# Performance work log

Measured on AMD Instinct MI355X. Metric: run time of the kernel, lower is better.

Reference implementation:

```python
import jax, jax.numpy as jnp
import numpy as np

B, S, H = 2, 2048, 4096          # batch, seq_len, hidden_size
NH, NKV, D = 32, 8, 128          # query heads, kv heads (GQA), head_dim
WINDOW = 1024                    # sliding window size
EPS = 1e-5
THETA = 10000.0


def setup_inputs() -> dict:
    key = jax.random.key(0)
    ks = jax.random.split(key, 5)
    w = lambda k, shape: jax.random.normal(k, shape, jnp.float32) * 0.02
    return {
        "hidden_states": jax.random.normal(ks[0], (B, S, H), jnp.float32),
        "wq": w(ks[1], (H, NH * D)),
        "wk": w(ks[2], (H, NKV * D)),
        "wv": w(ks[3], (H, NKV * D)),
        "wo": w(ks[4], (NH * D, H)),
        "q_norm_w": jnp.ones((D,), jnp.float32),
        "k_norm_w": jnp.ones((D,), jnp.float32),
    }


def _rmsnorm(x, w):
    # Exaone4RMSNorm over the last (head_dim) axis
    var = jnp.mean(jnp.square(x.astype(jnp.float32)), axis=-1, keepdims=True)
    return (x * jax.lax.rsqrt(var + EPS)).astype(x.dtype) * w


def _rotate_half(x):
    x1, x2 = jnp.split(x, 2, axis=-1)
    return jnp.concatenate([-x2, x1], axis=-1)


def reference(hidden_states, wq, wk, wv, wo, q_norm_w, k_norm_w):
    # QKV projections (no bias)
    q = (hidden_states @ wq).reshape(B, S, NH, D)
    k = (hidden_states @ wk).reshape(B, S, NKV, D)
    v = (hidden_states @ wv).reshape(B, S, NKV, D)
    # per-head QK RMSNorm, then [B, h, S, D] layout
    q = _rmsnorm(q, q_norm_w).transpose(0, 2, 1, 3)
    k = _rmsnorm(k, k_norm_w).transpose(0, 2, 1, 3)
    v = v.transpose(0, 2, 1, 3)
    # RoPE (applied on sliding-window layers in EXAONE4)
    pos = jnp.arange(S)
    inv_freq = 1.0 / (THETA ** (jnp.arange(0, D, 2, dtype=jnp.float32) / D))
    freqs = pos[:, None].astype(jnp.float32) * inv_freq[None, :]   # [S, D/2]
    emb = jnp.concatenate([freqs, freqs], axis=-1)                 # [S, D]
    cos, sin = jnp.cos(emb), jnp.sin(emb)
    q = q * cos + _rotate_half(q) * sin
    k = k * cos + _rotate_half(k) * sin
    # GQA: repeat kv heads to match query heads
    k = jnp.repeat(k, NH // NKV, axis=1)
    v = jnp.repeat(v, NH // NKV, axis=1)
    # SDPA with causal sliding-window mask: q_pos - WINDOW < k_pos <= q_pos
    scores = jnp.einsum('bhqd,bhkd->bhqk', q, k) / jnp.sqrt(jnp.float32(D))
    diff = pos[:, None] - pos[None, :]
    mask = (diff >= 0) & (diff < WINDOW)
    scores = jnp.where(mask, scores, jnp.finfo(scores.dtype).min)
    probs = jax.nn.softmax(scores, axis=-1)
    out = jnp.einsum('bhqk,bhkd->bhqd', probs, v)
    out = out.transpose(0, 2, 1, 3).reshape(B, S, NH * D)
    return out @ wo
```

## Files before the change

### kernel.cpp

```cpp
#include <hip/hip_runtime.h>
#include <hip/hip_bf16.h>

#define B_ 2
#define S_ 2048
#define H_ 4096
#define NH_ 32
#define NKV_ 8
#define D_ 128
#define WINDOW_ 1024
#define EPS_ 1e-5f
#define M_ (B_*S_)
#define NQKV_ ((NH_ + 2*NKV_) * D_)

typedef __attribute__((ext_vector_type(8))) __bf16 bf16x8;
typedef __attribute__((ext_vector_type(4))) float f32x4;
typedef __attribute__((ext_vector_type(16))) float f32x16;

__device__ __forceinline__ unsigned short f2bf(float f) {
  union { __hip_bfloat16 h; unsigned short us; } cv;
  cv.h = __float2bfloat16(f);
  return cv.us;
}
__device__ __forceinline__ float bf2f(unsigned short u) {
  union { __hip_bfloat16 h; unsigned short us; } cv;
  cv.us = u;
  return __bfloat162float(cv.h);
}

__device__ __forceinline__ void gload16(const unsigned short* g, unsigned short* l) {
  __builtin_amdgcn_global_load_lds(
      (const __attribute__((address_space(1))) unsigned int*)(const void*)g,
      (__attribute__((address_space(3))) unsigned int*)(void*)l, 16, 0, 0);
}

__global__ __launch_bounds__(256) void transpose_convert(
    const float* __restrict__ in, unsigned short* __restrict__ out, int K, int N) {
  __shared__ float tile[32][33];
  const int n0 = blockIdx.x * 32, k0 = blockIdx.y * 32;
  const int t = threadIdx.x;
  #pragma unroll
  for (int i = 0; i < 4; ++i) {
    int e = i * 256 + t; int r = e >> 5, c = e & 31;
    tile[r][c] = in[(size_t)(k0 + r) * N + n0 + c];
  }
  __syncthreads();
  #pragma unroll
  for (int i = 0; i < 4; ++i) {
    int e = i * 256 + t; int r = e >> 5, c = e & 31;
    out[(size_t)(n0 + r) * K + k0 + c] = f2bf(tile[c][r]);
  }
}

__global__ __launch_bounds__(256) void convert_bf16_kernel(
    const float* __restrict__ in, unsigned short* __restrict__ out, int n4) {
  int i = blockIdx.x * 256 + threadIdx.x;
  if (i >= n4) return;
  float4 v = ((const float4*)in)[i];
  ushort4 o;
  o.x = f2bf(v.x); o.y = f2bf(v.y); o.z = f2bf(v.z); o.w = f2bf(v.w);
  ((ushort4*)out)[i] = o;
}

template <bool OUT_BF16>
__global__ __launch_bounds__(512) void gemm9(
    const unsigned short* __restrict__ A, const unsigned short* __restrict__ Bt,
    void* __restrict__ Cout, int N, int K) {
  __shared__ __align__(16) unsigned short lds[2][2][16384];
  const int tid = threadIdx.x;
  const int wave = tid >> 6, lane = tid & 63;
  const int l15 = lane & 15, l16 = lane >> 4;
  const int m0 = blockIdx.y * 256, n0 = blockIdx.x * 256;
  const int wmi = wave >> 2, wni = wave & 3;

  const unsigned short* asrc[4];
  const unsigned short* bsrc[4];
  #pragma unroll
  for (int it = 0; it < 4; ++it) {
    const int d = it * 512 + tid;
    const int row = d >> 3, cis = (d & 7) ^ (row & 7);
    asrc[it] = A + (size_t)(m0 + row) * K + cis * 8;
    bsrc[it] = Bt + (size_t)(n0 + row) * K + cis * 8;
  }

  int offA[2][8], offB[2][4];
  #pragma unroll
  for (int kk = 0; kk < 2; ++kk) {
    #pragma unroll
    for (int mi = 0; mi < 8; ++mi) {
      const int row = wmi * 128 + mi * 16 + l15;
      offA[kk][mi] = row * 64 + ((kk * 4 + l16) ^ (row & 7)) * 8;
    }
    #pragma unroll
    for (int ni = 0; ni < 4; ++ni) {
      const int row = wni * 64 + ni * 16 + l15;
      offB[kk][ni] = row * 64 + ((kk * 4 + l16) ^ (row & 7)) * 8;
    }
  }

  f32x4 acc[8][4];
  #pragma unroll
  for (int mi = 0; mi < 8; ++mi)
    #pragma unroll
    for (int ni = 0; ni < 4; ++ni) acc[mi][ni] = (f32x4){0.f, 0.f, 0.f, 0.f};

#define STG(buf, kt)                                                         \
  { _Pragma("unroll") for (int it = 0; it < 4; ++it) {                       \
      const int dst = it * 4096 + wave * 512;                                \
      gload16(asrc[it] + (size_t)(kt) * 64, &lds[buf][0][dst]);              \
      gload16(bsrc[it] + (size_t)(kt) * 64, &lds[buf][1][dst]);              \
    } }

#define PHASE_MFMA(MOFF)                                                     \
  asm volatile("s_waitcnt lgkmcnt(0)" ::: "memory");                         \
  __builtin_amdgcn_sched_barrier(0);                                         \
  __builtin_amdgcn_s_setprio(1);                                             \
  _Pragma("unroll") for (int i = 0; i < 4; ++i)                              \
    _Pragma("unroll") for (int j = 0; j < 4; ++j)                            \
      acc[(MOFF) + i][j] = __builtin_amdgcn_mfma_f32_16x16x32_bf16(          \
          av[i], bv[j], acc[(MOFF) + i][j], 0, 0, 0);                        \
  __builtin_amdgcn_s_setprio(0);                                             \
  __builtin_amdgcn_sched_barrier(0);

  const int nk = K >> 6;
  STG(0, 0)
  for (int t = 0; t < nk; ++t) {
    const int cur = t & 1;
    if (t + 1 < nk) {
      STG(cur ^ 1, t + 1)
      asm volatile("s_waitcnt vmcnt(8)" ::: "memory");
    } else {
      asm volatile("s_waitcnt vmcnt(0)" ::: "memory");
    }
    __builtin_amdgcn_sched_barrier(0);
    __builtin_amdgcn_s_barrier();
    __builtin_amdgcn_sched_barrier(0);
    const unsigned short* as = lds[cur][0];
    const unsigned short* bs = lds[cur][1];
    bf16x8 av[4], bv[4];
    #pragma unroll
    for (int i = 0; i < 4; ++i) av[i] = *(const bf16x8*)&as[offA[0][i]];
    #pragma unroll
    for (int j = 0; j < 4; ++j) bv[j] = *(const bf16x8*)&bs[offB[0][j]];
    PHASE_MFMA(0)
    __builtin_amdgcn_s_barrier();
    #pragma unroll
    for (int i = 0; i < 4; ++i) av[i] = *(const bf16x8*)&as[offA[0][i + 4]];
    PHASE_MFMA(4)
    __builtin_amdgcn_s_barrier();
    #pragma unroll
    for (int i = 0; i < 4; ++i) av[i] = *(const bf16x8*)&as[offA[1][i]];
    #pragma unroll
    for (int j = 0; j < 4; ++j) bv[j] = *(const bf16x8*)&bs[offB[1][j]];
    PHASE_MFMA(0)
    __builtin_amdgcn_s_barrier();
    #pragma unroll
    for (int i = 0; i < 4; ++i) av[i] = *(const bf16x8*)&as[offA[1][i + 4]];
    PHASE_MFMA(4)
    __builtin_amdgcn_s_barrier();
    __builtin_amdgcn_sched_barrier(0);
  }
#undef STG
#undef PHASE_MFMA

  #pragma unroll
  for (int mi = 0; mi < 8; ++mi) {
    #pragma unroll
    for (int ni = 0; ni < 4; ++ni) {
      const int col = n0 + wni * 64 + ni * 16 + l15;
      #pragma unroll
      for (int j = 0; j < 4; ++j) {
        const int row = m0 + wmi * 128 + mi * 16 + l16 * 4 + j;
        if (OUT_BF16)
          ((unsigned short*)Cout)[(size_t)row * N + col] = f2bf(acc[mi][ni][j]);
        else
          ((float*)Cout)[(size_t)row * N + col] = acc[mi][ni][j];
      }
    }
  }
}

__global__ __launch_bounds__(256) void norm_rope_kernel(
    const unsigned short* __restrict__ QKVg,
    const float* __restrict__ qw, const float* __restrict__ kw,
    unsigned short* __restrict__ Qr, unsigned short* __restrict__ Kr) {
  const int bs = blockIdx.x;
  const int b = bs >> 11, s = bs & (S_ - 1);
  const int wave = threadIdx.x >> 6, lane = threadIdx.x & 63;

  float invf = 1.0f / powf(10000.0f, (float)lane * (1.0f / 64.0f));
  float sn, cs;
  sincosf((float)s * invf, &sn, &cs);

  const unsigned short* row = QKVg + (size_t)bs * NQKV_;
  const float qwa = qw[lane], qwb = qw[lane + 64];
  const float kwa = kw[lane], kwb = kw[lane + 64];
  const float scale = 0.08838834764831845f;

  for (int h = wave; h < NH_; h += 4) {
    float x0 = bf2f(row[h * D_ + lane]);
    float x1 = bf2f(row[h * D_ + 64 + lane]);
    float ss = x0 * x0 + x1 * x1;
    #pragma unroll
    for (int o = 32; o >= 1; o >>= 1) ss += __shfl_xor(ss, o);
    float r = rsqrtf(ss * (1.0f / 128.0f) + EPS_);
    x0 *= r * qwa; x1 *= r * qwb;
    float o0 = (x0 * cs - x1 * sn) * scale;
    float o1 = (x1 * cs + x0 * sn) * scale;
    size_t off = (((size_t)b * NH_ + h) * S_ + s) * D_;
    Qr[off + lane] = f2bf(o0);
    Qr[off + 64 + lane] = f2bf(o1);
  }
  for (int h = wave; h < NKV_; h += 4) {
    float x0 = bf2f(row[NH_ * D_ + h * D_ + lane]);
    float x1 = bf2f(row[NH_ * D_ + h * D_ + 64 + lane]);
    float ss = x0 * x0 + x1 * x1;
    #pragma unroll
    for (int o = 32; o >= 1; o >>= 1) ss += __shfl_xor(ss, o);
    float r = rsqrtf(ss * (1.0f / 128.0f) + EPS_);
    x0 *= r * kwa; x1 *= r * kwb;
    float o0 = x0 * cs - x1 * sn;
    float o1 = x1 * cs + x0 * sn;
    size_t off = (((size_t)b * NKV_ + h) * S_ + s) * D_;
    Kr[off + lane] = f2bf(o0);
    Kr[off + 64 + lane] = f2bf(o1);
  }
}

__global__ __launch_bounds__(256) void vtrans_kernel(
    const unsigned short* __restrict__ QKVg, unsigned short* __restrict__ Vt) {
  __shared__ unsigned short t[64][65];
  const int s0 = blockIdx.x * 64, d0 = blockIdx.y * 64;
  const int bh = blockIdx.z;
  const int b = bh >> 3, hk = bh & 7;
  const int tid = threadIdx.x;
  #pragma unroll
  for (int i = 0; i < 16; ++i) {
    int e = i * 256 + tid; int sr = e >> 6, dc = e & 63;
    t[sr][dc] = QKVg[(size_t)(b * S_ + s0 + sr) * NQKV_ + (NH_ + NKV_) * D_ + hk * D_ + d0 + dc];
  }
  __syncthreads();
  #pragma unroll
  for (int i = 0; i < 16; ++i) {
    int e = i * 256 + tid; int dr = e >> 6, sc = e & 63;
    Vt[((size_t)bh * D_ + d0 + dr) * S_ + s0 + sc] = t[sc][dr];
  }
}

__global__ __launch_bounds__(512) void attn_kernel(
    const unsigned short* __restrict__ Qr, const unsigned short* __restrict__ Kr,
    const unsigned short* __restrict__ Vt, unsigned short* __restrict__ Out) {
  const int q0 = blockIdx.x * 256;
  const int h = blockIdx.y, b = blockIdx.z, hk = h >> 2;
  const int tid = threadIdx.x;
  const int wave = tid >> 6, lane = tid & 63;
  const int l31 = lane & 31, hi = lane >> 5;
  const int qw0 = q0 + wave * 32;
  const int qpos = qw0 + l31;

  __shared__ __align__(16) unsigned short Ks[64 * 128];
  __shared__ __align__(16) unsigned short Vs[128 * 64];

  bf16x8 qf[8];
  {
    const unsigned short* qp = Qr + (((size_t)b * NH_ + h) * S_ + qpos) * D_ + hi * 8;
    #pragma unroll
    for (int ds = 0; ds < 8; ++ds) qf[ds] = *(const bf16x8*)(qp + ds * 16);
  }

  f32x16 o[4];
  #pragma unroll
  for (int i = 0; i < 4; ++i)
    #pragma unroll
    for (int j = 0; j < 16; ++j) o[i][j] = 0.f;
  float mrun = -1e30f, lrun = 0.f;

  const size_t kbase = ((size_t)b * NKV_ + hk) * S_;
  const size_t vbase = ((size_t)b * NKV_ + hk) * D_;

  const int ktlo = (q0 > 1023) ? ((q0 - 1023) & ~63) : 0;
  const int kthi = (q0 + 255) & ~63;
  const int wlo = (qw0 > 1023) ? ((qw0 - 1023) & ~63) : 0;
  const int whi = (qw0 + 31) & ~63;

  for (int kt = ktlo; kt <= kthi; kt += 64) {
    __syncthreads();
    #pragma unroll
    for (int it = 0; it < 2; ++it) {
      const int cb = it * 512 + wave * 64;
      const int c = cb + lane;
      const int rk = c >> 4, sk = c & 15;
      gload16(Kr + (kbase + kt + rk) * D_ + ((sk ^ (rk & 7)) * 8), Ks + (size_t)cb * 8);
      const int rv = c >> 3, sv = c & 7;
      gload16(Vt + (vbase + rv) * S_ + kt + ((sv ^ (rv & 7)) * 8), Vs + (size_t)cb * 8);
    }
    __syncthreads();
    if (kt < wlo || kt > whi) continue;

    f32x16 s0, s1;
    #pragma unroll
    for (int j = 0; j < 16; ++j) { s0[j] = 0.f; s1[j] = 0.f; }
    __builtin_amdgcn_s_setprio(1);
    #pragma unroll
    for (int ds = 0; ds < 8; ++ds) {
      const int g = ((ds * 2 + hi) ^ (l31 & 7)) * 8;
      bf16x8 k0 = *(const bf16x8*)&Ks[l31 * 128 + g];
      bf16x8 k1 = *(const bf16x8*)&Ks[(l31 + 32) * 128 + g];
      s0 = __builtin_amdgcn_mfma_f32_32x32x16_bf16(k0, qf[ds], s0, 0, 0, 0);
      s1 = __builtin_amdgcn_mfma_f32_32x32x16_bf16(k1, qf[ds], s1, 0, 0, 0);
    }
    __builtin_amdgcn_s_setprio(0);

    const bool fullValid = (kt + 63 <= qw0) && (kt >= qw0 - 992);
    if (!fullValid) {
      const int d0 = qpos - kt;
      #pragma unroll
      for (int r = 0; r < 16; ++r) {
        const int koff = (r & 3) + 8 * (r >> 2) + 4 * hi;
        if ((unsigned)(d0 - koff) >= (unsigned)WINDOW_) s0[r] = -1e30f;
        if ((unsigned)(d0 - koff - 32) >= (unsigned)WINDOW_) s1[r] = -1e30f;
      }
    }

    float pm = -1e30f;
    #pragma unroll
    for (int r = 0; r < 16; ++r) pm = fmaxf(pm, fmaxf(s0[r], s1[r]));
    pm = fmaxf(pm, __shfl_xor(pm, 32));
    const float mnew = fmaxf(mrun, pm);
    const float scl = __expf(mrun - mnew);
    mrun = mnew;
    float ts = 0.f;
    #pragma unroll
    for (int r = 0; r < 16; ++r) {
      s0[r] = __expf(s0[r] - mnew); ts += s0[r];
      s1[r] = __expf(s1[r] - mnew); ts += s1[r];
    }
    ts += __shfl_xor(ts, 32);
    lrun = lrun * scl + ts;
    #pragma unroll
    for (int i = 0; i < 4; ++i)
      #pragma unroll
      for (int j = 0; j < 16; ++j) o[i][j] *= scl;

    unsigned pw[2][2][4];
    #pragma unroll
    for (int t2 = 0; t2 < 2; ++t2) {
      const f32x16 sv = t2 ? s1 : s0;
      #pragma unroll
      for (int sub = 0; sub < 2; ++sub) {
        const int bs4 = sub * 8;
        unsigned A0 = ((unsigned)f2bf(sv[bs4 + 1]) << 16) | f2bf(sv[bs4 + 0]);
        unsigned A1 = ((unsigned)f2bf(sv[bs4 + 3]) << 16) | f2bf(sv[bs4 + 2]);
        unsigned B0 = ((unsigned)f2bf(sv[bs4 + 5]) << 16) | f2bf(sv[bs4 + 4]);
        unsigned B1 = ((unsigned)f2bf(sv[bs4 + 7]) << 16) | f2bf(sv[bs4 + 6]);
        unsigned sA0 = __shfl_xor(A0, 32), sA1 = __shfl_xor(A1, 32);
        unsigned sB0 = __shfl_xor(B0, 32), sB1 = __shfl_xor(B1, 32);
        pw[t2][sub][0] = hi ? sB0 : A0;
        pw[t2][sub][1] = hi ? sB1 : A1;
        pw[t2][sub][2] = hi ? B0 : sA0;
        pw[t2][sub][3] = hi ? B1 : sA1;
      }
    }

    __builtin_amdgcn_s_setprio(1);
    #pragma unroll
    for (int t2 = 0; t2 < 2; ++t2)
      #pragma unroll
      for (int sub = 0; sub < 2; ++sub) {
        union { unsigned u[4]; bf16x8 v; } pb;
        pb.u[0] = pw[t2][sub][0]; pb.u[1] = pw[t2][sub][1];
        pb.u[2] = pw[t2][sub][2]; pb.u[3] = pw[t2][sub][3];
        #pragma unroll
        for (int dt = 0; dt < 4; ++dt) {
          const int rr = dt * 32 + l31;
          const int g = ((t2 * 4 + sub * 2 + hi) ^ (rr & 7)) * 8;
          bf16x8 vf = *(const bf16x8*)&Vs[rr * 64 + g];
          o[dt] = __builtin_amdgcn_mfma_f32_32x32x16_bf16(vf, pb.v, o[dt], 0, 0, 0);
        }
      }
    __builtin_amdgcn_s_setprio(0);
  }

  const float inv = 1.0f / lrun;
  unsigned short* op = Out + (size_t)(b * S_ + qpos) * (NH_ * D_) + h * D_;
  #pragma unroll
  for (int dt = 0; dt < 4; ++dt)
    #pragma unroll
    for (int g = 0; g < 4; ++g) {
      const int r = g * 4;
      uint2 val;
      val.x = ((unsigned)f2bf(o[dt][r + 1] * inv) << 16) | f2bf(o[dt][r + 0] * inv);
      val.y = ((unsigned)f2bf(o[dt][r + 3] * inv) << 16) | f2bf(o[dt][r + 2] * inv);
      *(uint2*)(op + dt * 32 + 8 * g + 4 * hi) = val;
    }
}

extern "C" void kernel_launch(void* const* d_in, const int* in_sizes, int n_in,
                              void* d_out, int out_size, void* d_ws, size_t ws_size,
                              hipStream_t stream) {
  const float* hidden = (const float*)d_in[0];
  const float* wq = (const float*)d_in[1];
  const float* wk = (const float*)d_in[2];
  const float* wv = (const float*)d_in[3];
  const float* wo = (const float*)d_in[4];
  const float* qw = (const float*)d_in[5];
  const float* kw = (const float*)d_in[6];
  float* out = (float*)d_out;

  char* ws = (char*)d_ws;
  unsigned short* wqkv = (unsigned short*)(ws);
  unsigned short* kr   = (unsigned short*)(ws);
  unsigned short* vt   = (unsigned short*)(ws + ((size_t)8 << 20));
  unsigned short* attn = (unsigned short*)(ws + ((size_t)16 << 20));
  unsigned short* qkvg = (unsigned short*)(ws + ((size_t)48 << 20));
  unsigned short* wot  = (unsigned short*)(ws + ((size_t)48 << 20));
  unsigned short* hb   = (unsigned short*)d_out;
  unsigned short* qr   = (unsigned short*)d_out + ((size_t)16 << 20);

  transpose_convert<<<dim3(NH_ * D_ / 32, H_ / 32), 256, 0, stream>>>(wq, wqkv, H_, NH_ * D_);
  transpose_convert<<<dim3(NKV_ * D_ / 32, H_ / 32), 256, 0, stream>>>(
      wk, wqkv + (size_t)NH_ * D_ * H_, H_, NKV_ * D_);
  transpose_convert<<<dim3(NKV_ * D_ / 32, H_ / 32), 256, 0, stream>>>(
      wv, wqkv + (size_t)(NH_ + NKV_) * D_ * H_, H_, NKV_ * D_);

  convert_bf16_kernel<<<(M_ * H_ / 4 + 255) / 256, 256, 0, stream>>>(hidden, hb, M_ * H_ / 4);

  gemm9<true><<<dim3(NQKV_ / 256, M_ / 256), 512, 0, stream>>>(hb, wqkv, qkvg, NQKV_, H_);

  norm_rope_kernel<<<M_, 256, 0, stream>>>(qkvg, qw, kw, qr, kr);

  vtrans_kernel<<<dim3(S_ / 64, D_ / 64, B_ * NKV_), 256, 0, stream>>>(qkvg, vt);

  transpose_convert<<<dim3(H_ / 32, H_ / 32), 256, 0, stream>>>(wo, wot, NH_ * D_, H_);

  attn_kernel<<<dim3(S_ / 256, NH_, B_), 512, 0, stream>>>(qr, kr, vt, attn);

  gemm9<false><<<dim3(H_ / 256, M_ / 256), 512, 0, stream>>>(attn, wot, out, H_, H_);
}
```

Baseline: 572.6 us.

## Interleave GEMM prefetch loads across MFMA phases and add lazy softmax rescaling

```diff
diff --git a/kernel.cpp b/kernel.cpp
--- a/kernel.cpp
+++ b/kernel.cpp
@@ -62,7 +62,7 @@
 }
 
 template <bool OUT_BF16>
-__global__ __launch_bounds__(512) void gemm9(
+__global__ __launch_bounds__(512) void gemm10(
     const unsigned short* __restrict__ A, const unsigned short* __restrict__ Bt,
     void* __restrict__ Cout, int N, int K) {
   __shared__ __align__(16) unsigned short lds[2][2][16384];
@@ -102,13 +102,6 @@
   for (int mi = 0; mi < 8; ++mi)
     #pragma unroll
     for (int ni = 0; ni < 4; ++ni) acc[mi][ni] = (f32x4){0.f, 0.f, 0.f, 0.f};
-
-#define STG(buf, kt)                                                         \
-  { _Pragma("unroll") for (int it = 0; it < 4; ++it) {                       \
-      const int dst = it * 4096 + wave * 512;                                \
-      gload16(asrc[it] + (size_t)(kt) * 64, &lds[buf][0][dst]);              \
-      gload16(bsrc[it] + (size_t)(kt) * 64, &lds[buf][1][dst]);              \
-    } }
 
 #define PHASE_MFMA(MOFF)                                                     \
   asm volatile("s_waitcnt lgkmcnt(0)" ::: "memory");                         \
@@ -121,45 +114,74 @@
   __builtin_amdgcn_s_setprio(0);                                             \
   __builtin_amdgcn_sched_barrier(0);
 
+  #pragma unroll
+  for (int it = 0; it < 4; ++it) {
+    gload16(asrc[it], &lds[0][0][it * 4096 + wave * 512]);
+    gload16(bsrc[it], &lds[0][1][it * 4096 + wave * 512]);
+  }
+  asm volatile("s_waitcnt vmcnt(0)" ::: "memory");
+  __builtin_amdgcn_sched_barrier(0);
+  __builtin_amdgcn_s_barrier();
+
   const int nk = K >> 6;
-  STG(0, 0)
   for (int t = 0; t < nk; ++t) {
-    const int cur = t & 1;
-    if (t + 1 < nk) {
-      STG(cur ^ 1, t + 1)
-      asm volatile("s_waitcnt vmcnt(8)" ::: "memory");
-    } else {
-      asm volatile("s_waitcnt vmcnt(0)" ::: "memory");
-    }
-    __builtin_amdgcn_sched_barrier(0);
-    __builtin_amdgcn_s_barrier();
-    __builtin_amdgcn_sched_barrier(0);
+    const int cur = t & 1, nxt = cur ^ 1;
     const unsigned short* as = lds[cur][0];
     const unsigned short* bs = lds[cur][1];
+    const bool dostg = (t + 1 < nk);
+    const size_t ko = (size_t)(t + 1) * 64;
     bf16x8 av[4], bv[4];
+
     #pragma unroll
     for (int i = 0; i < 4; ++i) av[i] = *(const bf16x8*)&as[offA[0][i]];
     #pragma unroll
     for (int j = 0; j < 4; ++j) bv[j] = *(const bf16x8*)&bs[offB[0][j]];
+    if (dostg) {
+      gload16(asrc[0] + ko, &lds[nxt][0][0 * 4096 + wave * 512]);
+      gload16(asrc[1] + ko, &lds[nxt][0][1 * 4096 + wave * 512]);
+    }
+    __builtin_amdgcn_sched_barrier(0);
+    __builtin_amdgcn_s_barrier();
     PHASE_MFMA(0)
     __builtin_amdgcn_s_barrier();
+
     #pragma unroll
     for (int i = 0; i < 4; ++i) av[i] = *(const bf16x8*)&as[offA[0][i + 4]];
+    if (dostg) {
+      gload16(asrc[2] + ko, &lds[nxt][0][2 * 4096 + wave * 512]);
+      gload16(asrc[3] + ko, &lds[nxt][0][3 * 4096 + wave * 512]);
+    }
+    __builtin_amdgcn_sched_barrier(0);
+    __builtin_amdgcn_s_barrier();
     PHASE_MFMA(4)
     __builtin_amdgcn_s_barrier();
+
     #pragma unroll
     for (int i = 0; i < 4; ++i) av[i] = *(const bf16x8*)&as[offA[1][i]];
     #pragma unroll
     for (int j = 0; j < 4; ++j) bv[j] = *(const bf16x8*)&bs[offB[1][j]];
+    if (dostg) {
+      gload16(bsrc[0] + ko, &lds[nxt][1][0 * 4096 + wave * 512]);
+      gload16(bsrc[1] + ko, &lds[nxt][1][1 * 4096 + wave * 512]);
+    }
+    __builtin_amdgcn_sched_barrier(0);
+    __builtin_amdgcn_s_barrier();
     PHASE_MFMA(0)
     __builtin_amdgcn_s_barrier();
+
     #pragma unroll
     for (int i = 0; i < 4; ++i) av[i] = *(const bf16x8*)&as[offA[1][i + 4]];
+    if (dostg) {
+      gload16(bsrc[2] + ko, &lds[nxt][1][2 * 4096 + wave * 512]);
+      gload16(bsrc[3] + ko, &lds[nxt][1][3 * 4096 + wave * 512]);
+    }
+    __builtin_amdgcn_sched_barrier(0);
+    __builtin_amdgcn_s_barrier();
     PHASE_MFMA(4)
-    __builtin_amdgcn_s_barrier();
+    asm volatile("s_waitcnt vmcnt(0)" ::: "memory");
     __builtin_amdgcn_sched_barrier(0);
-  }
-#undef STG
+    __builtin_amdgcn_s_barrier();
+  }
 #undef PHASE_MFMA
 
   #pragma unroll
@@ -325,21 +347,24 @@
     #pragma unroll
     for (int r = 0; r < 16; ++r) pm = fmaxf(pm, fmaxf(s0[r], s1[r]));
     pm = fmaxf(pm, __shfl_xor(pm, 32));
-    const float mnew = fmaxf(mrun, pm);
-    const float scl = __expf(mrun - mnew);
-    mrun = mnew;
+    if (!__all(pm - mrun <= 8.f)) {
+      const float mnew = fmaxf(mrun, pm);
+      const float scl = __expf(mrun - mnew);
+      mrun = mnew;
+      lrun *= scl;
+      #pragma unroll
+      for (int i = 0; i < 4; ++i)
+        #pragma unroll
+        for (int j = 0; j < 16; ++j) o[i][j] *= scl;
+    }
     float ts = 0.f;
     #pragma unroll
     for (int r = 0; r < 16; ++r) {
-      s0[r] = __expf(s0[r] - mnew); ts += s0[r];
-      s1[r] = __expf(s1[r] - mnew); ts += s1[r];
+      s0[r] = __expf(s0[r] - mrun); ts += s0[r];
+      s1[r] = __expf(s1[r] - mrun); ts += s1[r];
     }
     ts += __shfl_xor(ts, 32);
-    lrun = lrun * scl + ts;
-    #pragma unroll
-    for (int i = 0; i < 4; ++i)
-      #pragma unroll
-      for (int j = 0; j < 16; ++j) o[i][j] *= scl;
+    lrun += ts;
 
     unsigned pw[2][2][4];
     #pragma unroll
@@ -424,7 +449,7 @@
 
   convert_bf16_kernel<<<(M_ * H_ / 4 + 255) / 256, 256, 0, stream>>>(hidden, hb, M_ * H_ / 4);
 
-  gemm9<true><<<dim3(NQKV_ / 256, M_ / 256), 512, 0, stream>>>(hb, wqkv, qkvg, NQKV_, H_);
+  gemm10<true><<<dim3(NQKV_ / 256, M_ / 256), 512, 0, stream>>>(hb, wqkv, qkvg, NQKV_, H_);
 
   norm_rope_kernel<<<M_, 256, 0, stream>>>(qkvg, qw, kw, qr, kr);
 
@@ -434,5 +459,5 @@
 
   attn_kernel<<<dim3(S_ / 256, NH_, B_), 512, 0, stream>>>(qr, kr, vt, attn);
 
-  gemm9<false><<<dim3(H_ / 256, M_ / 256), 512, 0, stream>>>(attn, wot, out, H_, H_);
-}
+  gemm10<false><<<dim3(H_ / 256, M_ / 256), 512, 0, stream>>>(attn, wot, out, H_, H_);
+}
```

Measured after the change: 545.9 us. 4.7% less time.
